# Performance work log

Hardware: AMD Instinct MI355X
Metric: run time of the kernel (lower is better)

Reference implementation:

```python
import jax, jax.numpy as jnp
import numpy as np

RADIUS = 0.15
NSAMPLE = 128
NPOINT = 128
EPS = 1e-5  # BatchNorm eps (eval mode, running_mean=0, running_var=1)


def _bn(x, g, b):
    shape = (1, -1) + (1,) * (x.ndim - 2)
    return x * (g / jnp.sqrt(1.0 + EPS)).reshape(shape) + b.reshape(shape)


def _fps(x, npoint):
    # farthest point sampling; x: (Bk, N, 3) -> (Bk, npoint) int32
    Bn, N, _ = x.shape

    def step(carry, _):
        dist, far = carry
        c = jnp.take_along_axis(x, far[:, None, None], 1)  # (Bk,1,3)
        d = jnp.sum((x - c) ** 2, -1)
        dist = jnp.minimum(dist, d)
        return (dist, jnp.argmax(dist, -1).astype(jnp.int32)), far

    init = (jnp.full((Bn, N), 1e10, x.dtype), jnp.zeros((Bn,), jnp.int32))
    _, idxs = jax.lax.scan(step, init, None, length=npoint)
    return idxs.T  # (Bk, npoint)


def _sa_module(x, f, mlp):
    # PointnetSAModuleVotes: FPS -> ball query -> group (use_xyz, normalize_xyz)
    # -> shared MLP (conv2d 1x1 + BN + ReLU) -> max over nsample.
    Bk, M, _ = x.shape
    fps_idx = _fps(x, NPOINT)
    new_xyz = jnp.take_along_axis(x, fps_idx[..., None], 1)  # (Bk,np,3)
    d2 = jnp.sum((new_xyz[:, :, None, :] - x[:, None, :, :]) ** 2, -1)  # (Bk,np,M)
    cand = jnp.where(d2 < RADIUS ** 2, jnp.arange(M)[None, None, :], M)
    cand = jnp.sort(cand, -1)[..., :NSAMPLE]  # first nsample in-radius indices
    first = cand[..., :1]
    first = jnp.where(first == M, 0, first)
    idx = jnp.where(cand == M, first, cand)  # (Bk,np,ns), pad with first valid
    gx = jnp.take_along_axis(x, idx.reshape(Bk, -1)[..., None], 1).reshape(Bk, NPOINT, NSAMPLE, 3)
    gxn = (gx - new_xyz[:, :, None, :]) / RADIUS  # normalize_xyz=True
    gf = jnp.take_along_axis(f[:, :, None, :], idx[:, None, :, :], 3)  # (Bk,C,np,ns)
    h = jnp.concatenate([gxn.transpose(0, 3, 1, 2), gf], 1)  # (Bk, C+3, np, ns)
    for (w, b, g, be) in mlp:
        h = jax.nn.relu(_bn(jnp.einsum('oc,bcps->bops', w, h) + b[None, :, None, None], g, be))
    return new_xyz, h.max(-1)  # (Bk,np,3), (Bk,128,np)


def setup_inputs() -> dict:
    key = jax.random.key(0)
    ks = iter(jax.random.split(key, 40))
    B, M, K, C = 2, 1024, 19, 256
    inp = {}
    inp['xyz'] = jax.random.normal(next(ks), (B, M, K, 3), jnp.float32)
    inp['features'] = jax.random.normal(next(ks), (B, C, K, M), jnp.float32)

    def conv_p(prefix, cin, cout):
        inp[prefix + '_w'] = jax.random.normal(next(ks), (cout, cin), jnp.float32) * (1.0 / np.sqrt(cin))
        inp[prefix + '_b'] = jax.random.normal(next(ks), (cout,), jnp.float32) * 0.02
        inp[prefix + '_g'] = 1.0 + 0.1 * jax.random.normal(next(ks), (cout,), jnp.float32)
        inp[prefix + '_be'] = 0.02 * jax.random.normal(next(ks), (cout,), jnp.float32)

    conv_p('m1', C + 3, 128)  # use_xyz -> 259 in-channels
    conv_p('m2', 128, 128)
    conv_p('m3', 128, 128)
    conv_p('c1', 128, 128)
    conv_p('c2', 128, 128)
    inp['op_w'] = jax.random.normal(next(ks), (K, 5, 128), jnp.float32) * (1.0 / np.sqrt(128))
    inp['op_b'] = jax.random.normal(next(ks), (K, 5), jnp.float32) * 0.02
    return inp


def reference(xyz, features, m1_w, m1_b, m1_g, m1_be, m2_w, m2_b, m2_g, m2_be,
              m3_w, m3_b, m3_g, m3_be, c1_w, c1_b, c1_g, c1_be,
              c2_w, c2_b, c2_g, c2_be, op_w, op_b):
    B, M, K, _ = xyz.shape
    C = features.shape[1]
    # fold vote_factor k into the batch dim (all per-k SA/conv weights are shared)
    x = xyz.transpose(0, 2, 1, 3).reshape(B * K, M, 3)
    f = features.transpose(0, 2, 1, 3).reshape(B * K, C, M)
    mlp = [(m1_w, m1_b, m1_g, m1_be), (m2_w, m2_b, m2_g, m2_be), (m3_w, m3_b, m3_g, m3_be)]
    new_xyz, feat = _sa_module(x, f, mlp)
    net = jax.nn.relu(_bn(jnp.einsum('oc,bcp->bop', c1_w, feat) + c1_b[None, :, None], c1_g, c1_be))
    net = jax.nn.relu(_bn(jnp.einsum('oc,bcp->bop', c2_w, net) + c2_b[None, :, None], c2_g, c2_be))
    net = net.reshape(B, K, 128, NPOINT)
    # per-k output conv (conv_op ModuleList), 128 -> 2+3
    out = jnp.einsum('koc,bkcp->bkop', op_w, net) + op_b[None, :, :, None]
    net_t = out.transpose(0, 1, 3, 2)  # (B,K,np,5)
    agg_xyz = new_xyz.reshape(B, K, NPOINT, 3)
    center = agg_xyz + net_t[..., 2:5]  # decode_scores_
    scores = jnp.concatenate([net_t[..., :2], center], -1)  # obj(2) + center(3)
    return scores, agg_xyz, feat.reshape(B, K, 128, NPOINT)
```

## Files before the change

kernel.cpp:

```cpp
#include <hip/hip_runtime.h>
#include <math.h>

#define NBK   38

#define OFF_XC    0u
#define OFF_NXYZ  466944u
#define OFF_BIDX  525312u
#define OFF_W1F   3015680u
#define OFF_PREP  22938624u
#define OFF_WF    22955008u
#define OFF_CNT   23348224u

#define OUT_AGG   24320
#define OUT_FEAT  38912

typedef short bf16x8 __attribute__((ext_vector_type(8)));
typedef float f32x4  __attribute__((ext_vector_type(4)));
typedef int   v4i    __attribute__((ext_vector_type(4)));
typedef int   v2i    __attribute__((ext_vector_type(2)));

__device__ __forceinline__ float dist2f(float a0, float a1, float a2,
                                        float b0, float b1, float b2) {
#pragma clang fp contract(off)
  float d0 = a0 - b0;
  float d1 = a1 - b1;
  float d2 = a2 - b2;
  return d0 * d0 + d1 * d1 + d2 * d2;
}

__device__ __forceinline__ void split2rn(float v, unsigned& sh, unsigned& sm) {
  unsigned u = __float_as_uint(v);
  unsigned rh = (u + 0x7fffu + ((u >> 16) & 1u)) & 0xffff0000u;
  sh = rh >> 16;
  float r1 = v - __uint_as_float(rh);
  unsigned u1 = __float_as_uint(r1);
  unsigned rm = (u1 + 0x7fffu + ((u1 >> 16) & 1u)) & 0xffff0000u;
  sm = rm >> 16;
}

#define DPP_FMAX_STEP(v, ctrl)                                                 \
  {                                                                            \
    int _s = __builtin_amdgcn_update_dpp(__float_as_int(v), __float_as_int(v), \
                                         (ctrl), 0xf, 0xf, false);             \
    (v) = fmaxf((v), __int_as_float(_s));                                      \
  }

__global__ __launch_bounds__(512, 2) void front_kernel(
    const float* __restrict__ xyz, const float* __restrict__ feats,
    const float* __restrict__ m1w, const float* __restrict__ m1b,
    const float* __restrict__ m1g, const float* __restrict__ m1be,
    const float* __restrict__ m2w, const float* __restrict__ m2b,
    const float* __restrict__ m2g, const float* __restrict__ m2be,
    const float* __restrict__ m3w, const float* __restrict__ m3b,
    const float* __restrict__ m3g, const float* __restrict__ m3be,
    const float* __restrict__ c1w, const float* __restrict__ c1b,
    const float* __restrict__ c1g, const float* __restrict__ c1be,
    const float* __restrict__ c2w, const float* __restrict__ c2b,
    const float* __restrict__ c2g, const float* __restrict__ c2be,
    float* __restrict__ xc, float* __restrict__ nxyz, float* __restrict__ agg,
    int* __restrict__ bidx, int* __restrict__ counts,
    float* __restrict__ W1f, short* __restrict__ Wf, float* __restrict__ prep)
{
  __shared__ __align__(16) char smem[32768];
  int bid = blockIdx.x, t = threadIdx.x;
  int wave = t >> 6, lane = t & 63;

  if (bid < NBK) {
    int bk = bid;
    int b = bk / 19, k = bk % 19;
    float4* sp4 = (float4*)smem;
    float4* scen4 = (float4*)(smem + 16384);

    for (int i = t; i < 1024; i += 512) {
      const float* src = xyz + ((size_t)((b * 1024 + i) * 19 + k)) * 3;
      float x0 = src[0], x1 = src[1], x2 = src[2];
      sp4[i] = make_float4(x0, x1, x2, 0.f);
      xc[(bk * 3 + 0) * 1024 + i] = x0;
      xc[(bk * 3 + 1) * 1024 + i] = x1;
      xc[(bk * 3 + 2) * 1024 + i] = x2;
    }
    __syncthreads();

    if (wave == 0) {
      float px[16], py[16], pz[16], dist[16];
#pragma unroll
      for (int j = 0; j < 16; ++j) {
        float4 p = sp4[(lane << 4) + j];
        px[j] = p.x; py[j] = p.y; pz[j] = p.z;
        dist[j] = 1e10f;
      }
#pragma unroll
      for (int j = 0; j < 16; ++j)
        asm volatile("" : "+v"(px[j]), "+v"(py[j]), "+v"(pz[j]));

      int far = 0;
      for (int it = 0; it < 128; ++it) {
        float4 c = sp4[far];
        if (lane == 0) scen4[it] = c;
#pragma unroll
        for (int j = 0; j < 16; ++j) {
          float d = dist2f(px[j], py[j], pz[j], c.x, c.y, c.z);
          dist[j] = fminf(dist[j], d);
        }
        float tv[8]; int tj[8];
#pragma unroll
        for (int i = 0; i < 8; ++i) {
          bool L = dist[2 * i] >= dist[2 * i + 1];
          tv[i] = L ? dist[2 * i] : dist[2 * i + 1];
          tj[i] = L ? (2 * i) : (2 * i + 1);
        }
#pragma unroll
        for (int s = 1; s < 8; s <<= 1) {
#pragma unroll
          for (int i = 0; i < 8; i += 2 * s) {
            bool L = tv[i] >= tv[i + s];
            tv[i] = L ? tv[i] : tv[i + s];
            tj[i] = L ? tj[i] : tj[i + s];
          }
        }
        float lmax = tv[0];
        float g = lmax;
        DPP_FMAX_STEP(g, 0x111);
        DPP_FMAX_STEP(g, 0x112);
        DPP_FMAX_STEP(g, 0x114);
        DPP_FMAX_STEP(g, 0x118);
        float r0 = __int_as_float(__builtin_amdgcn_readlane(__float_as_int(g), 15));
        float r1 = __int_as_float(__builtin_amdgcn_readlane(__float_as_int(g), 31));
        float r2 = __int_as_float(__builtin_amdgcn_readlane(__float_as_int(g), 47));
        float r3 = __int_as_float(__builtin_amdgcn_readlane(__float_as_int(g), 63));
        float gmax = fmaxf(fmaxf(r0, r1), fmaxf(r2, r3));
        unsigned long long mk = __ballot(lmax == gmax);
        int wl = (int)__builtin_ctzll(mk);
        far = __builtin_amdgcn_readlane((lane << 4) + tj[0], wl);
      }
    }
    __syncthreads();

    if (t < 384) {
      float v = ((const float*)scen4)[(t / 3) * 4 + (t % 3)];
      nxyz[bk * 384 + t] = v;
      agg[bk * 384 + t]  = v;
    }

    for (int p = wave * 16; p < wave * 16 + 16; ++p) {
      float4 cen = scen4[p];
      int* outp = bidx + ((size_t)(bk * 128 + p)) * 128;
      int count = 0, first = 0;
      bool got = false;
      for (int ch = 0; ch < 16 && count < 128; ++ch) {
        int m = (ch << 6) + lane;
        float4 pv = sp4[m];
        float d = dist2f(pv.x, pv.y, pv.z, cen.x, cen.y, cen.z);
        bool flag = d < 0.0225f;
        unsigned long long mask = __ballot(flag);
        if (!got && mask) { first = (ch << 6) + __builtin_ctzll(mask); got = true; }
        int pos = count + (int)__popcll(mask & ((1ull << lane) - 1ull));
        if (flag && pos < 128) outp[pos] = m;
        count += (int)__popcll(mask);
      }
      for (int j = count + lane; j < 128; j += 64) outp[j] = first;
      if (lane == 0) counts[bk * 128 + p] = count > 128 ? 128 : count;
    }
    return;
  }

  if (bid < 342) {
    short* ffrag = (short*)smem;
    if (t >= 256) {
      for (int i = 0; i < 8; ++i) __syncthreads();
      return;
    }
    int blk = bid - NBK;
    int bk = blk >> 3, m0 = (blk & 7) << 7;
    int b = bk / 19, k = bk % 19;
    int quad = lane >> 4, nl = lane & 15;
    int mloc = t & 127, chalf = t >> 7;
    int st_w = mloc >> 4, sl_w = mloc & 15;
    const float* fbase = feats + ((size_t)(b * 4864 + k)) * 1024 + m0 + mloc;

    f32x4 acc[2][8];
#pragma unroll
    for (int oi = 0; oi < 2; ++oi)
#pragma unroll
      for (int st = 0; st < 8; ++st) acc[oi][st] = (f32x4){0.f, 0.f, 0.f, 0.f};

    for (int ch = 0; ch < 4; ++ch) {
      int cbase = ch * 64 + chalf * 32;
#pragma unroll
      for (int g = 0; g < 4; ++g) {
        float v[8];
#pragma unroll
        for (int j = 0; j < 8; ++j)
          v[j] = fbase[(size_t)(cbase + g * 8 + j) * 19456];
        unsigned sh[8], sm[8];
#pragma unroll
        for (int j = 0; j < 8; ++j) split2rn(v[j], sh[j], sm[j]);
        int base = chalf * 4096 + st_w * 512 + (g * 16 + sl_w) * 8;
        v4i ph = {(int)(sh[0] | (sh[1] << 16)), (int)(sh[2] | (sh[3] << 16)),
                  (int)(sh[4] | (sh[5] << 16)), (int)(sh[6] | (sh[7] << 16))};
        *(v4i*)&ffrag[base] = ph;
        v4i pm = {(int)(sm[0] | (sm[1] << 16)), (int)(sm[2] | (sm[3] << 16)),
                  (int)(sm[4] | (sm[5] << 16)), (int)(sm[6] | (sm[7] << 16))};
        *(v4i*)&ffrag[base + 8192] = pm;
      }
      __syncthreads();
#pragma unroll
      for (int kkl = 0; kkl < 2; ++kkl) {
        int kk = ch * 2 + kkl;
        bf16x8 a[2][2];
#pragma unroll
        for (int oi = 0; oi < 2; ++oi) {
          int o_row = (wave * 2 + oi) * 16 + nl;
          const float* wsrc = m1w + o_row * 259 + 3 + kk * 32 + quad * 8;
          float wv[8];
#pragma unroll
          for (int j = 0; j < 8; ++j) wv[j] = wsrc[j];
          unsigned sh[8], sm[8];
#pragma unroll
          for (int j = 0; j < 8; ++j) split2rn(wv[j], sh[j], sm[j]);
          short ah[8], am[8];
#pragma unroll
          for (int j = 0; j < 8; ++j) { ah[j] = (short)sh[j]; am[j] = (short)sm[j]; }
          a[oi][0] = (bf16x8){ah[0], ah[1], ah[2], ah[3], ah[4], ah[5], ah[6], ah[7]};
          a[oi][1] = (bf16x8){am[0], am[1], am[2], am[3], am[4], am[5], am[6], am[7]};
        }
#pragma unroll
        for (int st = 0; st < 8; ++st) {
          const short* hb = ffrag + kkl * 4096 + st * 512 + lane * 8;
          bf16x8 b0 = *(const bf16x8*)hb;
          bf16x8 b1 = *(const bf16x8*)(hb + 8192);
#pragma unroll
          for (int oi = 0; oi < 2; ++oi) {
            f32x4 c = acc[oi][st];
            c = __builtin_amdgcn_mfma_f32_16x16x32_bf16(a[oi][1], b0, c, 0, 0, 0);
            c = __builtin_amdgcn_mfma_f32_16x16x32_bf16(a[oi][0], b1, c, 0, 0, 0);
            c = __builtin_amdgcn_mfma_f32_16x16x32_bf16(a[oi][0], b0, c, 0, 0, 0);
            acc[oi][st] = c;
          }
        }
      }
      __syncthreads();
    }
    float inv = 1.0f / sqrtf(1.0f + 1e-5f);
#pragma unroll
    for (int oi = 0; oi < 2; ++oi) {
      int o0 = (wave * 2 + oi) * 16 + quad * 4;
      float4 bb = *(const float4*)&m1b[o0];
      float4 gg = *(const float4*)&m1g[o0];
#pragma unroll
      for (int st = 0; st < 8; ++st) {
        int m_out = m0 + st * 16 + nl;
        f32x4 cc = acc[oi][st];
        float4 r;
        r.x = (cc[0] + bb.x) * (gg.x * inv);
        r.y = (cc[1] + bb.y) * (gg.y * inv);
        r.z = (cc[2] + bb.z) * (gg.z * inv);
        r.w = (cc[3] + bb.w) * (gg.w * inv);
        *(float4*)&W1f[((size_t)(bk * 1024 + m_out)) * 128 + o0] = r;
      }
    }
    return;
  }

  if (bid < 358) {
    int idx = (bid - 342) * 512 + t;
#pragma unroll
    for (int e = 0; e < 4; ++e) {
      int i = idx * 4 + e;
      int c = i & 127, o = (i >> 7) & 127, l = i >> 14;
      float w = (l ? m3w : m2w)[o * 128 + c];
      unsigned sh, sm;
      split2rn(w, sh, sm);
      int ot = o >> 4, mm = o & 15, kk = c >> 5, q = (c & 31) >> 3, j = c & 7;
      int within = (q * 16 + mm) * 8 + j;
      Wf[(((l * 2 + 0) * 4 + kk) * 8 + ot) * 512 + within] = (short)sh;
      Wf[(((l * 2 + 1) * 4 + kk) * 8 + ot) * 512 + within] = (short)sm;
    }
    return;
  }

  if (bid < 374) {
    int idx2 = (bid - 358) * 512 + t;
#pragma unroll
    for (int e = 0; e < 4; ++e) {
      int i = idx2 * 4 + e;
      int c = i & 127, o = (i >> 7) & 127, l = i >> 14;
      float w = (l ? c2w : c1w)[o * 128 + c];
      unsigned sh, sm;
      split2rn(w, sh, sm);
      int ot = o >> 4, mm = o & 15, kk = c >> 5, q = (c & 31) >> 3, j = c & 7;
      int within = (q * 16 + mm) * 8 + j;
      Wf[131072 + (((l * 2 + 0) * 4 + kk) * 8 + ot) * 512 + within] = (short)sh;
      Wf[131072 + (((l * 2 + 1) * 4 + kk) * 8 + ot) * 512 + within] = (short)sm;
    }
    return;
  }

  if (t < 128) {
    float inv = 1.0f / sqrtf(1.0f + 1e-5f);
    float a1 = m1g[t] * inv;
    prep[t] = a1;
    float a2 = m2g[t] * inv;  prep[256 + t] = a2;  prep[384 + t] = fmaf(m2b[t], a2, m2be[t]);
    float a3 = m3g[t] * inv;  prep[512 + t] = a3;  prep[640 + t] = fmaf(m3b[t], a3, m3be[t]);
    float ac1 = c1g[t] * inv; prep[768 + t] = ac1; prep[896 + t] = fmaf(c1b[t], ac1, c1be[t]);
    float ac2 = c2g[t] * inv; prep[1024 + t] = ac2; prep[1152 + t] = fmaf(c2b[t], ac2, c2be[t]);
    prep[1280 + 4 * t + 0] = m1w[t * 259 + 0] * a1;
    prep[1280 + 4 * t + 1] = m1w[t * 259 + 1] * a1;
    prep[1280 + 4 * t + 2] = m1w[t * 259 + 2] * a1;
    prep[1280 + 4 * t + 3] = m1be[t];
  }
}

__device__ __forceinline__ void mfma_layer(const short* __restrict__ Wf,
                                           const short* hfrag, int l,
                                           int wave, int lane, int nst_h,
                                           f32x4 acc[2][4])
{
#pragma unroll 1
  for (int kk = 0; kk < 4; ++kk) {
    bf16x8 a[2][2];
#pragma unroll
    for (int oi = 0; oi < 2; ++oi)
#pragma unroll
      for (int sp = 0; sp < 2; ++sp)
        a[oi][sp] = *(const bf16x8*)(Wf + (((l * 2 + sp) * 4 + kk) * 8 + (wave * 2 + oi)) * 512 + lane * 8);
    for (int st = 0; st < nst_h; ++st) {
      const short* hb = hfrag + kk * 2048 + st * 512 + lane * 8;
      bf16x8 b0 = *(const bf16x8*)(hb);
      bf16x8 b1 = *(const bf16x8*)(hb + 8192);
#pragma unroll
      for (int oi = 0; oi < 2; ++oi) {
        f32x4 c = acc[oi][st];
        c = __builtin_amdgcn_mfma_f32_16x16x32_bf16(a[oi][1], b0, c, 0, 0, 0);
        c = __builtin_amdgcn_mfma_f32_16x16x32_bf16(a[oi][0], b1, c, 0, 0, 0);
        c = __builtin_amdgcn_mfma_f32_16x16x32_bf16(a[oi][0], b0, c, 0, 0, 0);
        acc[oi][st] = c;
      }
    }
  }
}

__global__ __launch_bounds__(256, 3) void sa_kernel(
    const float* __restrict__ xc, const float* __restrict__ nxyz,
    const int* __restrict__ bidx, const int* __restrict__ counts,
    const float* __restrict__ W1f, const float* __restrict__ prep,
    const short* __restrict__ Wf, float* __restrict__ feat_out)
{
  __shared__ __align__(16) short hfrag[16384];
  __shared__ float pcs[512];
  __shared__ float sm[32 * 128];
  __shared__ float ccen[12];
  __shared__ int scnt[4];
  int gb = blockIdx.x, bk = gb >> 5, pb = (gb & 31) << 2;
  int t = threadIdx.x;
  int wave = t >> 6, lane = t & 63;
  int quad = lane >> 4, nl = lane & 15;

  pcs[t] = prep[1280 + t];
  pcs[256 + t] = prep[1536 + t];
  if (t < 4) scnt[t] = counts[bk * 128 + pb + t];
  if (t < 12) {
    int bb = t / 3, c = t % 3;
    ccen[t] = nxyz[(bk * 128 + pb + bb) * 3 + c];
  }
  __syncthreads();
  int n0 = (scnt[0] + 15) >> 4, n1 = (scnt[1] + 15) >> 4;
  int n2 = (scnt[2] + 15) >> 4, n3 = (scnt[3] + 15) >> 4;
  int pf1 = n0, pf2 = n0 + n1, pf3 = n0 + n1 + n2, T = n0 + n1 + n2 + n3;

  for (int q0 = 0; q0 < T; q0 += 4) {
    int nst_h = T - q0;
    if (nst_h > 4) nst_h = 4;
    {
      int cg = wave;
      int st = lane >> 4, sl = lane & 15;
      if (st < nst_h) {
        int q = q0 + st;
        int bq = (q >= pf1) + (q >= pf2) + (q >= pf3);
        int tstart = (bq == 0) ? 0 : (bq == 1) ? pf1 : (bq == 2) ? pf2 : pf3;
        int tslot = q - tstart;
        int m = bidx[((size_t)(bk * 128 + pb + bq)) * 128 + tslot * 16 + sl];
        float cen0 = ccen[bq * 3 + 0], cen1 = ccen[bq * 3 + 1], cen2 = ccen[bq * 3 + 2];
        float g0 = (xc[(bk * 3 + 0) * 1024 + m] - cen0) * (1.0f / 0.15f);
        float g1 = (xc[(bk * 3 + 1) * 1024 + m] - cen1) * (1.0f / 0.15f);
        float g2 = (xc[(bk * 3 + 2) * 1024 + m] - cen2) * (1.0f / 0.15f);
        const float4* wrow = (const float4*)(W1f + ((size_t)(bk * 1024 + m)) * 128 + cg * 32);
        const float4* pcp = (const float4*)pcs + cg * 32;
#pragma unroll
        for (int g = 0; g < 4; ++g) {
          float4 wva = wrow[g * 2], wvb = wrow[g * 2 + 1];
          float wv[8] = {wva.x, wva.y, wva.z, wva.w, wvb.x, wvb.y, wvb.z, wvb.w};
          unsigned sh[8], smv[8];
#pragma unroll
          for (int e = 0; e < 8; ++e) {
            float4 pc = pcp[g * 8 + e];
            float hv = fmaxf(wv[e] + pc.x * g0 + pc.y * g1 + pc.z * g2 + pc.w, 0.f);
            split2rn(hv, sh[e], smv[e]);
          }
          int base = (cg * 4 + st) * 512 + (g * 16 + sl) * 8;
          v4i ph = {(int)(sh[0] | (sh[1] << 16)), (int)(sh[2] | (sh[3] << 16)),
                    (int)(sh[4] | (sh[5] << 16)), (int)(sh[6] | (sh[7] << 16))};
          *(v4i*)&hfrag[base] = ph;
          v4i pm = {(int)(smv[0] | (smv[1] << 16)), (int)(smv[2] | (smv[3] << 16)),
                    (int)(smv[4] | (smv[5] << 16)), (int)(smv[6] | (smv[7] << 16))};
          *(v4i*)&hfrag[base + 8192] = pm;
        }
      }
    }
    __syncthreads();

    f32x4 acc[2][4];
#pragma unroll
    for (int oi = 0; oi < 2; ++oi)
#pragma unroll
      for (int st = 0; st < 4; ++st) acc[oi][st] = (f32x4){0.f, 0.f, 0.f, 0.f};
    mfma_layer(Wf, hfrag, 0, wave, lane, nst_h, acc);
    __syncthreads();

#pragma unroll
    for (int oi = 0; oi < 2; ++oi) {
      int o0 = (wave * 2 + oi) * 16 + quad * 4;
      float4 al = *(const float4*)&prep[256 + o0];
      float4 be = *(const float4*)&prep[384 + o0];
      int kk2 = o0 >> 5, g2 = (o0 & 31) >> 3, j0 = o0 & 7;
      for (int st = 0; st < nst_h; ++st) {
        f32x4 cc = acc[oi][st];
        float v0 = fmaxf(fmaf(cc[0], al.x, be.x), 0.f);
        float v1 = fmaxf(fmaf(cc[1], al.y, be.y), 0.f);
        float v2 = fmaxf(fmaf(cc[2], al.z, be.z), 0.f);
        float v3 = fmaxf(fmaf(cc[3], al.w, be.w), 0.f);
        unsigned h0, m0_, h1, m1_, h2, m2_, h3, m3_;
        split2rn(v0, h0, m0_); split2rn(v1, h1, m1_);
        split2rn(v2, h2, m2_); split2rn(v3, h3, m3_);
        int base = (kk2 * 4 + st) * 512 + (g2 * 16 + nl) * 8 + j0;
        v2i w0 = {(int)(h0 | (h1 << 16)), (int)(h2 | (h3 << 16))};
        *(v2i*)&hfrag[base] = w0;
        v2i w1 = {(int)(m0_ | (m1_ << 16)), (int)(m2_ | (m3_ << 16))};
        *(v2i*)&hfrag[base + 8192] = w1;
      }
    }
    __syncthreads();

#pragma unroll
    for (int oi = 0; oi < 2; ++oi)
#pragma unroll
      for (int st = 0; st < 4; ++st) acc[oi][st] = (f32x4){0.f, 0.f, 0.f, 0.f};
    mfma_layer(Wf, hfrag, 1, wave, lane, nst_h, acc);

#pragma unroll
    for (int oi = 0; oi < 2; ++oi) {
      int o0 = (wave * 2 + oi) * 16 + quad * 4;
      float4 al = *(const float4*)&prep[512 + o0];
      float4 be = *(const float4*)&prep[640 + o0];
      for (int st = 0; st < nst_h; ++st) {
        f32x4 cc = acc[oi][st];
        float v[4];
        v[0] = fmaxf(fmaf(cc[0], al.x, be.x), 0.f);
        v[1] = fmaxf(fmaf(cc[1], al.y, be.y), 0.f);
        v[2] = fmaxf(fmaf(cc[2], al.z, be.z), 0.f);
        v[3] = fmaxf(fmaf(cc[3], al.w, be.w), 0.f);
#pragma unroll
        for (int r = 0; r < 4; ++r) {
          float x = v[r];
          x = fmaxf(x, __shfl_xor(x, 1));
          x = fmaxf(x, __shfl_xor(x, 2));
          x = fmaxf(x, __shfl_xor(x, 4));
          x = fmaxf(x, __shfl_xor(x, 8));
          if (nl == 0) sm[(q0 + st) * 128 + o0 + r] = x;
        }
      }
    }
    __syncthreads();
  }

#pragma unroll
  for (int e = t; e < 512; e += 256) {
    int bb = e >> 7, o = e & 127;
    int qs = (bb == 0) ? 0 : (bb == 1) ? pf1 : (bb == 2) ? pf2 : pf3;
    int nq = (bb == 0) ? n0 : (bb == 1) ? n1 : (bb == 2) ? n2 : n3;
    float v = sm[qs * 128 + o];
    for (int q = 1; q < nq; ++q) v = fmaxf(v, sm[(qs + q) * 128 + o]);
    feat_out[(((size_t)bk) << 14) + (o << 7) + pb + bb] = v;
  }
}

__global__ __launch_bounds__(256) void head_kernel(const float* __restrict__ featg,
    const float* __restrict__ prep, const short* __restrict__ Wf,
    const float* __restrict__ nxyz, const float* __restrict__ opw,
    const float* __restrict__ opb, float* __restrict__ scores)
{
  __shared__ __align__(16) short hfrag[16384];
  __shared__ float hplain[128 * 65];
  int bk = blockIdx.x >> 1, p0 = (blockIdx.x & 1) << 6;
  int t = threadIdx.x;
  int wave = t >> 6, lane = t & 63;
  int quad = lane >> 4, nl = lane & 15;
  const short* WC = Wf + 131072;

  {
    int cg = wave;
    int st = lane >> 4, sl = lane & 15;
    const float* fb = featg + (bk << 14) + p0 + lane;
#pragma unroll
    for (int g = 0; g < 4; ++g) {
      float v[8];
#pragma unroll
      for (int e = 0; e < 8; ++e)
        v[e] = fb[(cg * 32 + g * 8 + e) << 7];
      unsigned sh[8], sm[8];
#pragma unroll
      for (int e = 0; e < 8; ++e) split2rn(v[e], sh[e], sm[e]);
      int base = (cg * 4 + st) * 512 + (g * 16 + sl) * 8;
      v4i ph = {(int)(sh[0] | (sh[1] << 16)), (int)(sh[2] | (sh[3] << 16)),
                (int)(sh[4] | (sh[5] << 16)), (int)(sh[6] | (sh[7] << 16))};
      *(v4i*)&hfrag[base] = ph;
      v4i pm = {(int)(sm[0] | (sm[1] << 16)), (int)(sm[2] | (sm[3] << 16)),
                (int)(sm[4] | (sm[5] << 16)), (int)(sm[6] | (sm[7] << 16))};
      *(v4i*)&hfrag[base + 8192] = pm;
    }
  }
  __syncthreads();

  f32x4 acc[2][4];
#pragma unroll
  for (int oi = 0; oi < 2; ++oi)
#pragma unroll
    for (int st = 0; st < 4; ++st) acc[oi][st] = (f32x4){0.f, 0.f, 0.f, 0.f};
  mfma_layer(WC, hfrag, 0, wave, lane, 4, acc);
  __syncthreads();

#pragma unroll
  for (int oi = 0; oi < 2; ++oi) {
    int o0 = (wave * 2 + oi) * 16 + quad * 4;
    float4 al = *(const float4*)&prep[768 + o0];
    float4 be = *(const float4*)&prep[896 + o0];
    int kk2 = o0 >> 5, g2 = (o0 & 31) >> 3, j0 = o0 & 7;
#pragma unroll
    for (int st = 0; st < 4; ++st) {
      f32x4 cc = acc[oi][st];
      float v0 = fmaxf(fmaf(cc[0], al.x, be.x), 0.f);
      float v1 = fmaxf(fmaf(cc[1], al.y, be.y), 0.f);
      float v2 = fmaxf(fmaf(cc[2], al.z, be.z), 0.f);
      float v3 = fmaxf(fmaf(cc[3], al.w, be.w), 0.f);
      unsigned h0, m0_, h1, m1_, h2, m2_, h3, m3_;
      split2rn(v0, h0, m0_); split2rn(v1, h1, m1_);
      split2rn(v2, h2, m2_); split2rn(v3, h3, m3_);
      int base = (kk2 * 4 + st) * 512 + (g2 * 16 + nl) * 8 + j0;
      v2i w0 = {(int)(h0 | (h1 << 16)), (int)(h2 | (h3 << 16))};
      *(v2i*)&hfrag[base] = w0;
      v2i w1 = {(int)(m0_ | (m1_ << 16)), (int)(m2_ | (m3_ << 16))};
      *(v2i*)&hfrag[base + 8192] = w1;
    }
  }
  __syncthreads();

#pragma unroll
  for (int oi = 0; oi < 2; ++oi)
#pragma unroll
    for (int st = 0; st < 4; ++st) acc[oi][st] = (f32x4){0.f, 0.f, 0.f, 0.f};
  mfma_layer(WC, hfrag, 1, wave, lane, 4, acc);

#pragma unroll
  for (int oi = 0; oi < 2; ++oi) {
    int o0 = (wave * 2 + oi) * 16 + quad * 4;
    float4 al = *(const float4*)&prep[1024 + o0];
    float4 be = *(const float4*)&prep[1152 + o0];
#pragma unroll
    for (int st = 0; st < 4; ++st) {
      f32x4 cc = acc[oi][st];
      int p = st * 16 + nl;
      hplain[(o0 + 0) * 65 + p] = fmaxf(fmaf(cc[0], al.x, be.x), 0.f);
      hplain[(o0 + 1) * 65 + p] = fmaxf(fmaf(cc[1], al.y, be.y), 0.f);
      hplain[(o0 + 2) * 65 + p] = fmaxf(fmaf(cc[2], al.z, be.z), 0.f);
      hplain[(o0 + 3) * 65 + p] = fmaxf(fmaf(cc[3], al.w, be.w), 0.f);
    }
  }
  __syncthreads();

  if (t < 64) {
    int p = t, k = bk % 19;
    float res[5];
#pragma unroll
    for (int j = 0; j < 5; ++j) {
      const float* wr = opw + ((size_t)(k * 5 + j)) * 128;
      float a = opb[k * 5 + j];
      for (int c = 0; c < 128; ++c) a = fmaf(wr[c], hplain[c * 65 + p], a);
      res[j] = a;
    }
    int pg = p0 + p;
    float a0 = nxyz[(bk * 128 + pg) * 3 + 0];
    float a1 = nxyz[(bk * 128 + pg) * 3 + 1];
    float a2 = nxyz[(bk * 128 + pg) * 3 + 2];
    float* sc = scores + ((size_t)(bk * 128 + pg)) * 5;
    sc[0] = res[0];
    sc[1] = res[1];
    sc[2] = a0 + res[2];
    sc[3] = a1 + res[3];
    sc[4] = a2 + res[4];
  }
}

extern "C" void kernel_launch(void* const* d_in, const int* in_sizes, int n_in,
                              void* d_out, int out_size, void* d_ws, size_t ws_size,
                              hipStream_t stream) {
  (void)in_sizes; (void)n_in; (void)out_size; (void)ws_size;
  const float* xyz  = (const float*)d_in[0];
  const float* fts  = (const float*)d_in[1];
  const float* m1w  = (const float*)d_in[2];
  const float* m1b  = (const float*)d_in[3];
  const float* m1g  = (const float*)d_in[4];
  const float* m1be = (const float*)d_in[5];
  const float* m2w  = (const float*)d_in[6];
  const float* m2b  = (const float*)d_in[7];
  const float* m2g  = (const float*)d_in[8];
  const float* m2be = (const float*)d_in[9];
  const float* m3w  = (const float*)d_in[10];
  const float* m3b  = (const float*)d_in[11];
  const float* m3g  = (const float*)d_in[12];
  const float* m3be = (const float*)d_in[13];
  const float* c1w  = (const float*)d_in[14];
  const float* c1b  = (const float*)d_in[15];
  const float* c1g  = (const float*)d_in[16];
  const float* c1be = (const float*)d_in[17];
  const float* c2w  = (const float*)d_in[18];
  const float* c2b  = (const float*)d_in[19];
  const float* c2g  = (const float*)d_in[20];
  const float* c2be = (const float*)d_in[21];
  const float* opw  = (const float*)d_in[22];
  const float* opb  = (const float*)d_in[23];

  float* out = (float*)d_out;
  char* ws = (char*)d_ws;
  float* xc   = (float*)(ws + OFF_XC);
  float* nxyz = (float*)(ws + OFF_NXYZ);
  int*   bidx = (int*)(ws + OFF_BIDX);
  float* W1f  = (float*)(ws + OFF_W1F);
  float* prep = (float*)(ws + OFF_PREP);
  short* Wf   = (short*)(ws + OFF_WF);
  int*   cnt  = (int*)(ws + OFF_CNT);

  hipLaunchKernelGGL(front_kernel, dim3(375), dim3(512), 0, stream,
                     xyz, fts, m1w, m1b, m1g, m1be, m2w, m2b, m2g, m2be,
                     m3w, m3b, m3g, m3be, c1w, c1b, c1g, c1be,
                     c2w, c2b, c2g, c2be,
                     xc, nxyz, out + OUT_AGG, bidx, cnt, W1f, Wf, prep);
  hipLaunchKernelGGL(sa_kernel, dim3(NBK * 32), dim3(256), 0, stream,
                     xc, nxyz, bidx, cnt, W1f, prep, Wf, out + OUT_FEAT);
  hipLaunchKernelGGL(head_kernel, dim3(NBK * 2), dim3(256), 0, stream,
                     out + OUT_FEAT, prep, Wf, nxyz, opw, opb, out);
}
```

Baseline: 297.6 us.

## Split FPS into its own kernel and carry winner coordinates through reduction

Farthest point sampling moves out of front_kernel into a separate fps_kernel of 38 blocks with 256 threads. front_kernel now reloads the points and sampled centers from the workspace before doing the ball query. The FPS loop now carries the winning point's coordinates through the argmax tree instead of its index, which removes the dependent LDS load of the next center from each iteration's critical path. The cost is an extra kernel launch, a serial dependency between the two kernels, and the loss of overlap between FPS and the weight-prep blocks of front_kernel.

After: 624.8 us. 110% more time.

```diff
diff --git a/kernel.cpp b/kernel.cpp
--- a/kernel.cpp
+++ b/kernel.cpp
@@ -44,6 +44,102 @@
                                          (ctrl), 0xf, 0xf, false);             \
     (v) = fmaxf((v), __int_as_float(_s));                                      \
   }
+
+__device__ __forceinline__ float readlane_f(float v, int l) {
+  return __int_as_float(__builtin_amdgcn_readlane(__float_as_int(v), l));
+}
+
+__global__ __launch_bounds__(256, 1) void fps_kernel(
+    const float* __restrict__ xyz, float* __restrict__ xc,
+    float* __restrict__ nxyz, float* __restrict__ agg)
+{
+  __shared__ __align__(16) float4 sp4[1024];
+  int bk = blockIdx.x;
+  int b = bk / 19, k = bk % 19;
+  int t = threadIdx.x, lane = t & 63, wave = t >> 6;
+
+  for (int i = t; i < 1024; i += 256) {
+    const float* src = xyz + ((size_t)((b * 1024 + i) * 19 + k)) * 3;
+    float x0 = src[0], x1 = src[1], x2 = src[2];
+    sp4[i] = make_float4(x0, x1, x2, 0.f);
+    xc[(bk * 3 + 0) * 1024 + i] = x0;
+    xc[(bk * 3 + 1) * 1024 + i] = x1;
+    xc[(bk * 3 + 2) * 1024 + i] = x2;
+  }
+  __syncthreads();
+  if (wave != 0) return;
+
+  float px[16], py[16], pz[16], dist[16];
+#pragma unroll
+  for (int j = 0; j < 16; ++j) {
+    float4 p = sp4[(lane << 4) + j];
+    px[j] = p.x; py[j] = p.y; pz[j] = p.z;
+    dist[j] = 1e10f;
+  }
+#pragma unroll
+  for (int j = 0; j < 16; ++j)
+    asm volatile("" : "+v"(px[j]), "+v"(py[j]), "+v"(pz[j]));
+
+  float cx = readlane_f(px[0], 0);
+  float cy = readlane_f(py[0], 0);
+  float cz = readlane_f(pz[0], 0);
+  if (lane == 0) {
+    nxyz[bk * 384 + 0] = cx; nxyz[bk * 384 + 1] = cy; nxyz[bk * 384 + 2] = cz;
+    agg[bk * 384 + 0] = cx;  agg[bk * 384 + 1] = cy;  agg[bk * 384 + 2] = cz;
+  }
+
+  for (int it = 1; it < 128; ++it) {
+#pragma unroll
+    for (int j = 0; j < 16; ++j) {
+      float d = dist2f(px[j], py[j], pz[j], cx, cy, cz);
+      dist[j] = fminf(dist[j], d);
+    }
+    float tv[8], tx[8], ty[8], tz[8];
+#pragma unroll
+    for (int i = 0; i < 8; ++i) {
+      bool L = dist[2 * i] >= dist[2 * i + 1];
+      tv[i] = L ? dist[2 * i] : dist[2 * i + 1];
+      tx[i] = L ? px[2 * i] : px[2 * i + 1];
+      ty[i] = L ? py[2 * i] : py[2 * i + 1];
+      tz[i] = L ? pz[2 * i] : pz[2 * i + 1];
+    }
+#pragma unroll
+    for (int s = 1; s < 8; s <<= 1) {
+#pragma unroll
+      for (int i = 0; i < 8; i += 2 * s) {
+        bool L = tv[i] >= tv[i + s];
+        tv[i] = L ? tv[i] : tv[i + s];
+        tx[i] = L ? tx[i] : tx[i + s];
+        ty[i] = L ? ty[i] : ty[i + s];
+        tz[i] = L ? tz[i] : tz[i + s];
+      }
+    }
+    float lmax = tv[0];
+    float g = lmax;
+    DPP_FMAX_STEP(g, 0x111);
+    DPP_FMAX_STEP(g, 0x112);
+    DPP_FMAX_STEP(g, 0x114);
+    DPP_FMAX_STEP(g, 0x118);
+    float r0 = readlane_f(g, 15);
+    float r1 = readlane_f(g, 31);
+    float r2 = readlane_f(g, 47);
+    float r3 = readlane_f(g, 63);
+    float gmax = fmaxf(fmaxf(r0, r1), fmaxf(r2, r3));
+    unsigned long long mk = __ballot(lmax == gmax);
+    int wl = (int)__builtin_ctzll(mk);
+    cx = readlane_f(tx[0], wl);
+    cy = readlane_f(ty[0], wl);
+    cz = readlane_f(tz[0], wl);
+    if (lane == 0) {
+      nxyz[bk * 384 + it * 3 + 0] = cx;
+      nxyz[bk * 384 + it * 3 + 1] = cy;
+      nxyz[bk * 384 + it * 3 + 2] = cz;
+      agg[bk * 384 + it * 3 + 0] = cx;
+      agg[bk * 384 + it * 3 + 1] = cy;
+      agg[bk * 384 + it * 3 + 2] = cz;
+    }
+  }
+}
 
 __global__ __launch_bounds__(512, 2) void front_kernel(
     const float* __restrict__ xyz, const float* __restrict__ feats,
@@ -57,7 +153,7 @@
     const float* __restrict__ c1g, const float* __restrict__ c1be,
     const float* __restrict__ c2w, const float* __restrict__ c2b,
     const float* __restrict__ c2g, const float* __restrict__ c2be,
-    float* __restrict__ xc, float* __restrict__ nxyz, float* __restrict__ agg,
+    float* __restrict__ xc, float* __restrict__ nxyz,
     int* __restrict__ bidx, int* __restrict__ counts,
     float* __restrict__ W1f, short* __restrict__ Wf, float* __restrict__ prep)
 {
@@ -67,80 +163,20 @@
 
   if (bid < NBK) {
     int bk = bid;
-    int b = bk / 19, k = bk % 19;
     float4* sp4 = (float4*)smem;
     float4* scen4 = (float4*)(smem + 16384);
 
     for (int i = t; i < 1024; i += 512) {
-      const float* src = xyz + ((size_t)((b * 1024 + i) * 19 + k)) * 3;
-      float x0 = src[0], x1 = src[1], x2 = src[2];
-      sp4[i] = make_float4(x0, x1, x2, 0.f);
-      xc[(bk * 3 + 0) * 1024 + i] = x0;
-      xc[(bk * 3 + 1) * 1024 + i] = x1;
-      xc[(bk * 3 + 2) * 1024 + i] = x2;
+      sp4[i] = make_float4(xc[(bk * 3 + 0) * 1024 + i],
+                           xc[(bk * 3 + 1) * 1024 + i],
+                           xc[(bk * 3 + 2) * 1024 + i], 0.f);
+    }
+    if (t < 128) {
+      scen4[t] = make_float4(nxyz[(bk * 128 + t) * 3 + 0],
+                             nxyz[(bk * 128 + t) * 3 + 1],
+                             nxyz[(bk * 128 + t) * 3 + 2], 0.f);
     }
     __syncthreads();
-
-    if (wave == 0) {
-      float px[16], py[16], pz[16], dist[16];
-#pragma unroll
-      for (int j = 0; j < 16; ++j) {
-        float4 p = sp4[(lane << 4) + j];
-        px[j] = p.x; py[j] = p.y; pz[j] = p.z;
-        dist[j] = 1e10f;
-      }
-#pragma unroll
-      for (int j = 0; j < 16; ++j)
-        asm volatile("" : "+v"(px[j]), "+v"(py[j]), "+v"(pz[j]));
-
-      int far = 0;
-      for (int it = 0; it < 128; ++it) {
-        float4 c = sp4[far];
-        if (lane == 0) scen4[it] = c;
-#pragma unroll
-        for (int j = 0; j < 16; ++j) {
-          float d = dist2f(px[j], py[j], pz[j], c.x, c.y, c.z);
-          dist[j] = fminf(dist[j], d);
-        }
-        float tv[8]; int tj[8];
-#pragma unroll
-        for (int i = 0; i < 8; ++i) {
-          bool L = dist[2 * i] >= dist[2 * i + 1];
-          tv[i] = L ? dist[2 * i] : dist[2 * i + 1];
-          tj[i] = L ? (2 * i) : (2 * i + 1);
-        }
-#pragma unroll
-        for (int s = 1; s < 8; s <<= 1) {
-#pragma unroll
-          for (int i = 0; i < 8; i += 2 * s) {
-            bool L = tv[i] >= tv[i + s];
-            tv[i] = L ? tv[i] : tv[i + s];
-            tj[i] = L ? tj[i] : tj[i + s];
-          }
-        }
-        float lmax = tv[0];
-        float g = lmax;
-        DPP_FMAX_STEP(g, 0x111);
-        DPP_FMAX_STEP(g, 0x112);
-        DPP_FMAX_STEP(g, 0x114);
-        DPP_FMAX_STEP(g, 0x118);
-        float r0 = __int_as_float(__builtin_amdgcn_readlane(__float_as_int(g), 15));
-        float r1 = __int_as_float(__builtin_amdgcn_readlane(__float_as_int(g), 31));
-        float r2 = __int_as_float(__builtin_amdgcn_readlane(__float_as_int(g), 47));
-        float r3 = __int_as_float(__builtin_amdgcn_readlane(__float_as_int(g), 63));
-        float gmax = fmaxf(fmaxf(r0, r1), fmaxf(r2, r3));
-        unsigned long long mk = __ballot(lmax == gmax);
-        int wl = (int)__builtin_ctzll(mk);
-        far = __builtin_amdgcn_readlane((lane << 4) + tj[0], wl);
-      }
-    }
-    __syncthreads();
-
-    if (t < 384) {
-      float v = ((const float*)scen4)[(t / 3) * 4 + (t % 3)];
-      nxyz[bk * 384 + t] = v;
-      agg[bk * 384 + t]  = v;
-    }
 
     for (int p = wave * 16; p < wave * 16 + 16; ++p) {
       float4 cen = scen4[p];
@@ -639,11 +675,13 @@
   short* Wf   = (short*)(ws + OFF_WF);
   int*   cnt  = (int*)(ws + OFF_CNT);
 
+  hipLaunchKernelGGL(fps_kernel, dim3(NBK), dim3(256), 0, stream,
+                     xyz, xc, nxyz, out + OUT_AGG);
   hipLaunchKernelGGL(front_kernel, dim3(375), dim3(512), 0, stream,
                      xyz, fts, m1w, m1b, m1g, m1be, m2w, m2b, m2g, m2be,
                      m3w, m3b, m3g, m3be, c1w, c1b, c1g, c1be,
                      c2w, c2b, c2g, c2be,
-                     xc, nxyz, out + OUT_AGG, bidx, cnt, W1f, Wf, prep);
+                     xc, nxyz, bidx, cnt, W1f, Wf, prep);
   hipLaunchKernelGGL(sa_kernel, dim3(NBK * 32), dim3(256), 0, stream,
                      xc, nxyz, bidx, cnt, W1f, prep, Wf, out + OUT_FEAT);
   hipLaunchKernelGGL(head_kernel, dim3(NBK * 2), dim3(256), 0, stream,
```
